# Performance work log

Measured on AMD Instinct MI355X. Metric: run time of the kernel, lower is better.

Reference implementation:

```python
import jax, jax.numpy as jnp
import numpy as np

IN_F, OUT_F = 4096, 4096
IN_Q, OUT_Q = IN_F // 4, OUT_F // 4


def setup_inputs() -> dict:
    key = jax.random.key(0)
    kx, kr, ki, kj, kk = jax.random.split(key, 5)
    std = 1.0 / np.sqrt(IN_F)
    x = jax.random.normal(kx, (4, 2048, IN_F), dtype=jnp.float32)
    Wr = std * jax.random.normal(kr, (OUT_Q, IN_Q), dtype=jnp.float32)
    Wi = std * jax.random.normal(ki, (OUT_Q, IN_Q), dtype=jnp.float32)
    Wj = std * jax.random.normal(kj, (OUT_Q, IN_Q), dtype=jnp.float32)
    Wk = std * jax.random.normal(kk, (OUT_Q, IN_Q), dtype=jnp.float32)
    bias = jnp.zeros((OUT_F,), dtype=jnp.float32)
    return {"x": x, "Wr": Wr, "Wi": Wi, "Wj": Wj, "Wk": Wk, "bias": bias}


def _hamilton_block(Wr, Wi, Wj, Wk):
    # Assemble the structured [4*out_q, 4*in_q] Hamilton block weight so the
    # whole op is ONE large GEMM instead of 16 small ones (same math).
    row_r = jnp.concatenate([Wr, -Wi, -Wj, -Wk], axis=1)
    row_i = jnp.concatenate([Wi,  Wr,  Wk, -Wj], axis=1)
    row_j = jnp.concatenate([Wj, -Wk,  Wr,  Wi], axis=1)
    row_k = jnp.concatenate([Wk,  Wj, -Wi,  Wr], axis=1)
    return jnp.concatenate([row_r, row_i, row_j, row_k], axis=0)  # [OUT_F, IN_F]


def reference(x, Wr, Wi, Wj, Wk, bias):
    W = _hamilton_block(Wr, Wi, Wj, Wk)
    # x: [B, S, IN_F] @ W.T -> [B, S, OUT_F]
    out = jnp.einsum('bsf,of->bso', x, W) + bias
    return out
```

## Files before the change

### kernel.cpp

```cpp
#include <hip/hip_runtime.h>
#include <hip/hip_bf16.h>


#define M_DIM 8192
#define N_DIM 4096
#define K_DIM 4096
#define BK 64
#define NT (K_DIM / BK)

typedef __attribute__((ext_vector_type(8))) short bf16x8;
typedef __attribute__((ext_vector_type(4))) float f32x4;
typedef __attribute__((ext_vector_type(8))) unsigned short ushort8;

static __device__ __forceinline__ unsigned short f2bf(float f) {
    unsigned int u = __float_as_uint(f);
    return (unsigned short)((u + 0x7fffu + ((u >> 16) & 1u)) >> 16);
}
static __device__ __forceinline__ unsigned short f2bf_sgn(float f, unsigned int sg) {
    unsigned int u = __float_as_uint(f) ^ sg;
    return (unsigned short)((u + 0x7fffu + ((u >> 16) & 1u)) >> 16);
}

__global__ __launch_bounds__(256) void cvt_x_kernel(const float* __restrict__ x,
                                                    unsigned short* __restrict__ xb) {
    int i = (blockIdx.x * 256 + threadIdx.x) * 8;
    f32x4 a = __builtin_nontemporal_load((const f32x4*)(x + i));
    f32x4 b = __builtin_nontemporal_load((const f32x4*)(x + i + 4));
    ushort8 o;
    o[0] = f2bf(a[0]); o[1] = f2bf(a[1]); o[2] = f2bf(a[2]); o[3] = f2bf(a[3]);
    o[4] = f2bf(b[0]); o[5] = f2bf(b[1]); o[6] = f2bf(b[2]); o[7] = f2bf(b[3]);
    *(ushort8*)(xb + i) = o;
}

__global__ __launch_bounds__(256) void prep_w_kernel(const float* __restrict__ Wr,
    const float* __restrict__ Wi, const float* __restrict__ Wj,
    const float* __restrict__ Wk, unsigned short* __restrict__ wb) {
    int row = blockIdx.x >> 1;
    int col = ((blockIdx.x & 1) * 256 + threadIdx.x) * 8;
    int p = row >> 10, q = col >> 10;
    int ci = p ^ q;
    const float* src = (ci == 0) ? Wr : (ci == 1) ? Wi : (ci == 2) ? Wj : Wk;
    unsigned int sg = ((0x428Eu >> (p * 4 + q)) & 1u) << 31;
    int so = (row & 1023) * 1024 + (col & 1023);
    f32x4 a = *(const f32x4*)(src + so);
    f32x4 b = *(const f32x4*)(src + so + 4);
    ushort8 o;
    o[0] = f2bf_sgn(a[0], sg); o[1] = f2bf_sgn(a[1], sg);
    o[2] = f2bf_sgn(a[2], sg); o[3] = f2bf_sgn(a[3], sg);
    o[4] = f2bf_sgn(b[0], sg); o[5] = f2bf_sgn(b[1], sg);
    o[6] = f2bf_sgn(b[2], sg); o[7] = f2bf_sgn(b[3], sg);
    *(ushort8*)(wb + row * 4096 + col) = o;
}

#define GLD16(gp, lp) __builtin_amdgcn_global_load_lds( \
    (const __attribute__((address_space(1))) void*)(gp), \
    (__attribute__((address_space(3))) void*)(lp), 16, 0, 0)

#define BAR() do { asm volatile("" ::: "memory"); \
                   __builtin_amdgcn_s_barrier(); \
                   asm volatile("" ::: "memory"); } while (0)
#define VM(n) asm volatile("s_waitcnt vmcnt(" #n ")" ::: "memory")

static __device__ __forceinline__ f32x4 MF(bf16x8 a, bf16x8 b, f32x4 c) {
    return __builtin_amdgcn_mfma_f32_16x16x32_bf16(a, b, c, 0, 0, 0);
}

__global__ __launch_bounds__(512, 2) void qgemm_bf16(
    const unsigned short* __restrict__ A, const unsigned short* __restrict__ B,
    const float* __restrict__ bias, float* __restrict__ out)
{
    __shared__ __align__(16) unsigned short Lsh[2][2][2][128 * 64];

    int bid = blockIdx.x;
    int cpx = gridDim.x >> 3;
    int wg  = (bid & 7) * cpx + (bid >> 3);
    int brow = (wg >> 4) * 256;
    int bcol = (wg & 15) * 256;

    int tid   = threadIdx.x;
    int lane  = tid & 63;
    int wid   = tid >> 6;
    int hA    = wid >> 2;
    int nb    = wid & 3;
    int hB    = nb >> 1;
    int rB0   = (nb & 1) << 6;
    int fr    = lane & 15;
    int fslot = lane >> 4;
    unsigned e = (unsigned)(fr & 7);

    const unsigned short* Ag = A + (size_t)brow * K_DIM;
    const unsigned short* Bg = B + (size_t)bcol * K_DIM;
    const char* LshB = (const char*)&Lsh[0][0][0][0];

    unsigned oA0 = (unsigned)hA * 16384u + (unsigned)fr * 128u
                 + ((((unsigned)fslot) ^ e) << 4);
    unsigned oA1 = oA0 ^ 64u;
    unsigned oB0 = 32768u + (unsigned)hB * 16384u
                 + (unsigned)(rB0 + fr) * 128u + ((((unsigned)fslot) ^ e) << 4);
    unsigned oB1 = oB0 ^ 64u;

    f32x4 acc[8][4] = {};

    auto stage = [&](int buf, int ab, int half, int t) {
        const unsigned short* g = (ab ? Bg : Ag) + (size_t)(half << 7) * K_DIM + t * BK;
        unsigned short* l = &Lsh[buf][ab][half][0];
        #pragma unroll
        for (int i = 0; i < 2; ++i) {
            int c = i * 512 + tid;
            int r = c >> 3, s = c & 7;
            GLD16(g + (size_t)r * K_DIM + ((s ^ (r & 7)) << 3), l + (c << 3));
        }
    };
    auto RD = [&](unsigned off) -> bf16x8 {
        return *(const bf16x8*)(LshB + off);
    };

#define CLUSTER(xa0, xa1, xb0, xb1, ra, rb)                                   \
    do {                                                                      \
        __builtin_amdgcn_s_setprio(1);                                        \
        _Pragma("unroll")                                                     \
        for (int ni = 0; ni < 4; ++ni) acc[ra][ni] = MF(xa0, bf0[ni], acc[ra][ni]); \
        _Pragma("unroll")                                                     \
        for (int ni = 0; ni < 4; ++ni) acc[rb][ni] = MF(xb0, bf0[ni], acc[rb][ni]); \
        _Pragma("unroll")                                                     \
        for (int ni = 0; ni < 4; ++ni) acc[ra][ni] = MF(xa1, bf1[ni], acc[ra][ni]); \
        _Pragma("unroll")                                                     \
        for (int ni = 0; ni < 4; ++ni) acc[rb][ni] = MF(xb1, bf1[ni], acc[rb][ni]); \
        __builtin_amdgcn_s_setprio(0);                                        \
    } while (0)

    stage(0, 0, 0, 0); stage(0, 0, 1, 0); stage(0, 1, 0, 0); stage(0, 1, 1, 0);
    stage(1, 1, 0, 1); stage(1, 1, 1, 1);
    VM(4); BAR();

    for (int t = 0; t < NT; ++t) {
        bf16x8 bf0[4], bf1[4];

        #pragma unroll
        for (int ni = 0; ni < 4; ++ni) {
            bf0[ni] = RD(oB0 + (unsigned)(ni * 2048));
            bf1[ni] = RD(oB1 + (unsigned)(ni * 2048));
        }
        bf16x8 p0a0 = RD(oA0), p0a1 = RD(oA1);
        bf16x8 p0b0 = RD(oA0 + 2048u), p0b1 = RD(oA1 + 2048u);
        if (t + 1 < NT) { stage((t & 1) ^ 1, 0, 0, t + 1); stage((t & 1) ^ 1, 0, 1, t + 1); }
        bf16x8 p1a0 = RD(oA0 + 4096u), p1a1 = RD(oA1 + 4096u);
        bf16x8 p1b0 = RD(oA0 + 6144u), p1b1 = RD(oA1 + 6144u);
        CLUSTER(p0a0, p0a1, p0b0, p0b1, 0, 1);
        BAR();

        if (t + 2 < NT) { stage(t & 1, 1, 0, t + 2); stage(t & 1, 1, 1, t + 2); }
        bf16x8 p2a0 = RD(oA0 + 8192u),  p2a1 = RD(oA1 + 8192u);
        bf16x8 p2b0 = RD(oA0 + 10240u), p2b1 = RD(oA1 + 10240u);
        CLUSTER(p1a0, p1a1, p1b0, p1b1, 2, 3);
        bf16x8 p3a0 = RD(oA0 + 12288u), p3a1 = RD(oA1 + 12288u);
        bf16x8 p3b0 = RD(oA0 + 14336u), p3b1 = RD(oA1 + 14336u);
        CLUSTER(p2a0, p2a1, p2b0, p2b1, 4, 5);
        CLUSTER(p3a0, p3a1, p3b0, p3b1, 6, 7);

        if (t < NT - 2) { VM(4); } else { VM(0); }
        BAR();
        oA0 ^= 0x10000u; oA1 ^= 0x10000u; oB0 ^= 0x10000u; oB1 ^= 0x10000u;
    }
#undef CLUSTER

    int cr = (lane >> 4) << 2;
    int cc = lane & 15;
    #pragma unroll
    for (int ni = 0; ni < 4; ++ni) {
        int col = bcol + nb * 64 + ni * 16 + cc;
        float bv = bias[col];
        #pragma unroll
        for (int mi = 0; mi < 8; ++mi) {
            int r0 = brow + hA * 128 + mi * 16 + cr;
            #pragma unroll
            for (int r = 0; r < 4; ++r)
                __builtin_nontemporal_store(acc[mi][ni][r] + bv,
                                            &out[(size_t)(r0 + r) * N_DIM + col]);
        }
    }
}

#define FBM 128
#define FBN 128
#define FBK 64
__global__ __launch_bounds__(256) void qgemm_fb(const float* __restrict__ x,
    const float* __restrict__ Wr, const float* __restrict__ Wi,
    const float* __restrict__ Wj, const float* __restrict__ Wk,
    const float* __restrict__ bias, float* __restrict__ out)
{
    __shared__ unsigned short As[FBM * FBK];
    __shared__ unsigned short Bs[FBN * FBK];

    int bid = blockIdx.x;
    int cpx = gridDim.x >> 3;
    int wg = (bid & 7) * cpx + (bid >> 3);
    int brow = (wg >> 5) * FBM;
    int bcol = (wg & 31) * FBN;

    int tid = threadIdx.x;
    int lane = tid & 63;
    int wv = tid >> 6;
    int wm = (wv >> 1) << 6;
    int wn = (wv & 1) << 6;
    int fr = lane & 15;
    int fk = (lane >> 4) << 3;

    int p = bcol >> 10;
    f32x4 acc[4][4] = {};

    for (int kt = 0; kt < K_DIM / FBK; ++kt) {
        int k0 = kt * FBK;
        int q = k0 >> 10;
        int ci = p ^ q;
        const float* wsrc = (ci == 0) ? Wr : (ci == 1) ? Wi : (ci == 2) ? Wj : Wk;
        unsigned int sg = ((0x428Eu >> (p * 4 + q)) & 1u) << 31;

        __syncthreads();
        #pragma unroll
        for (int i = 0; i < 4; ++i) {
            int c = i * 256 + tid;
            int row = c >> 3, colo = (c & 7) << 3;
            const float* s = x + (size_t)(brow + row) * K_DIM + k0 + colo;
            float4 a = *(const float4*)s;
            float4 b = *(const float4*)(s + 4);
            ushort8 o;
            o[0] = f2bf(a.x); o[1] = f2bf(a.y); o[2] = f2bf(a.z); o[3] = f2bf(a.w);
            o[4] = f2bf(b.x); o[5] = f2bf(b.y); o[6] = f2bf(b.z); o[7] = f2bf(b.w);
            *(ushort8*)(&As[c << 3]) = o;
        }
        #pragma unroll
        for (int i = 0; i < 4; ++i) {
            int c = i * 256 + tid;
            int row = c >> 3, colo = (c & 7) << 3;
            const float* s = wsrc + ((bcol + row) & 1023) * 1024 + ((k0 + colo) & 1023);
            float4 a = *(const float4*)s;
            float4 b = *(const float4*)(s + 4);
            ushort8 o;
            o[0] = f2bf_sgn(a.x, sg); o[1] = f2bf_sgn(a.y, sg);
            o[2] = f2bf_sgn(a.z, sg); o[3] = f2bf_sgn(a.w, sg);
            o[4] = f2bf_sgn(b.x, sg); o[5] = f2bf_sgn(b.y, sg);
            o[6] = f2bf_sgn(b.z, sg); o[7] = f2bf_sgn(b.w, sg);
            *(ushort8*)(&Bs[c << 3]) = o;
        }
        __syncthreads();

        #pragma unroll
        for (int ks = 0; ks < 2; ++ks) {
            bf16x8 af[4], bfr[4];
            #pragma unroll
            for (int m = 0; m < 4; ++m)
                af[m] = *(const bf16x8*)(&As[(wm + m * 16 + fr) * FBK + ks * 32 + fk]);
            #pragma unroll
            for (int n = 0; n < 4; ++n)
                bfr[n] = *(const bf16x8*)(&Bs[(wn + n * 16 + fr) * FBK + ks * 32 + fk]);
            #pragma unroll
            for (int m = 0; m < 4; ++m)
                #pragma unroll
                for (int n = 0; n < 4; ++n)
                    acc[m][n] = __builtin_amdgcn_mfma_f32_16x16x32_bf16(
                        af[m], bfr[n], acc[m][n], 0, 0, 0);
        }
    }

    int cr = (lane >> 4) << 2;
    int cc = lane & 15;
    #pragma unroll
    for (int n = 0; n < 4; ++n) {
        int col = bcol + wn + n * 16 + cc;
        float bv = bias[col];
        #pragma unroll
        for (int m = 0; m < 4; ++m) {
            int r0 = brow + wm + m * 16 + cr;
            #pragma unroll
            for (int r = 0; r < 4; ++r)
                out[(size_t)(r0 + r) * N_DIM + col] = acc[m][n][r] + bv;
        }
    }
}

extern "C" void kernel_launch(void* const* d_in, const int* in_sizes, int n_in,
                              void* d_out, int out_size, void* d_ws, size_t ws_size,
                              hipStream_t stream) {
    const float* x    = (const float*)d_in[0];
    const float* Wr   = (const float*)d_in[1];
    const float* Wi   = (const float*)d_in[2];
    const float* Wj   = (const float*)d_in[3];
    const float* Wk   = (const float*)d_in[4];
    const float* bias = (const float*)d_in[5];
    float* out = (float*)d_out;

    const size_t xb_bytes = (size_t)M_DIM * K_DIM * 2;
    const size_t wb_bytes = (size_t)N_DIM * K_DIM * 2;

    if (ws_size >= xb_bytes + wb_bytes) {
        unsigned short* xb = (unsigned short*)d_ws;
        unsigned short* wb = (unsigned short*)((char*)d_ws + xb_bytes);
        cvt_x_kernel<<<(M_DIM * K_DIM) / 2048, 256, 0, stream>>>(x, xb);
        prep_w_kernel<<<N_DIM * 2, 256, 0, stream>>>(Wr, Wi, Wj, Wk, wb);
        const int n_blocks = (M_DIM / 256) * (N_DIM / 256);
        qgemm_bf16<<<n_blocks, 512, 0, stream>>>(xb, wb, bias, out);
    } else {
        const int n_blocks = (M_DIM / FBM) * (N_DIM / FBN);
        qgemm_fb<<<n_blocks, 256, 0, stream>>>(x, Wr, Wi, Wj, Wk, bias, out);
    }
}
```

Baseline: 271.4 us.

## Use 16 waves per block with 64x64 per-wave tiles in bf16 GEMM

Doubles the workgroup to 1024 threads (16 waves in a 4x4 grid), so each wave computes a 64x64 output tile instead of 128x64, halving accumulator registers. LDS layout is flattened to full 256-row A/B tiles, staged by all threads, and A fragments are now read just in time inside each MFMA cluster. The goal is more waves to hide latency, at the cost of more LDS reads per MFMA and less register-level reuse. Launch bounds ask for 4 blocks per CU, which the 64 KB LDS footprint may not allow.

Measured after the change: 274.4 us. No clear change (+1.1%).

```diff
diff --git a/kernel.cpp b/kernel.cpp
--- a/kernel.cpp
+++ b/kernel.cpp
@@ -65,11 +65,11 @@
     return __builtin_amdgcn_mfma_f32_16x16x32_bf16(a, b, c, 0, 0, 0);
 }
 
-__global__ __launch_bounds__(512, 2) void qgemm_bf16(
+__global__ __launch_bounds__(1024, 4) void qgemm_bf16(
     const unsigned short* __restrict__ A, const unsigned short* __restrict__ B,
     const float* __restrict__ bias, float* __restrict__ out)
 {
-    __shared__ __align__(16) unsigned short Lsh[2][2][2][128 * 64];
+    __shared__ __align__(16) unsigned short Lsh[2][2][256 * 64];
 
     int bid = blockIdx.x;
     int cpx = gridDim.x >> 3;
@@ -80,33 +80,31 @@
     int tid   = threadIdx.x;
     int lane  = tid & 63;
     int wid   = tid >> 6;
-    int hA    = wid >> 2;
-    int nb    = wid & 3;
-    int hB    = nb >> 1;
-    int rB0   = (nb & 1) << 6;
+    int wm    = wid >> 2;
+    int wn    = wid & 3;
     int fr    = lane & 15;
     int fslot = lane >> 4;
     unsigned e = (unsigned)(fr & 7);
 
     const unsigned short* Ag = A + (size_t)brow * K_DIM;
     const unsigned short* Bg = B + (size_t)bcol * K_DIM;
-    const char* LshB = (const char*)&Lsh[0][0][0][0];
-
-    unsigned oA0 = (unsigned)hA * 16384u + (unsigned)fr * 128u
+    const char* LshB = (const char*)&Lsh[0][0][0];
+
+    unsigned oA0 = (unsigned)wm * 8192u + (unsigned)fr * 128u
                  + ((((unsigned)fslot) ^ e) << 4);
     unsigned oA1 = oA0 ^ 64u;
-    unsigned oB0 = 32768u + (unsigned)hB * 16384u
-                 + (unsigned)(rB0 + fr) * 128u + ((((unsigned)fslot) ^ e) << 4);
+    unsigned oB0 = 0x8000u + (unsigned)wn * 8192u + (unsigned)fr * 128u
+                 + ((((unsigned)fslot) ^ e) << 4);
     unsigned oB1 = oB0 ^ 64u;
 
-    f32x4 acc[8][4] = {};
-
-    auto stage = [&](int buf, int ab, int half, int t) {
-        const unsigned short* g = (ab ? Bg : Ag) + (size_t)(half << 7) * K_DIM + t * BK;
-        unsigned short* l = &Lsh[buf][ab][half][0];
+    f32x4 acc[4][4] = {};
+
+    auto stage = [&](int buf, int ab, int t) {
+        const unsigned short* g = (ab ? Bg : Ag) + t * BK;
+        unsigned short* l = &Lsh[buf][ab][0];
         #pragma unroll
         for (int i = 0; i < 2; ++i) {
-            int c = i * 512 + tid;
+            int c = i * 1024 + tid;
             int r = c >> 3, s = c & 7;
             GLD16(g + (size_t)r * K_DIM + ((s ^ (r & 7)) << 3), l + (c << 3));
         }
@@ -115,50 +113,40 @@
         return *(const bf16x8*)(LshB + off);
     };
 
-#define CLUSTER(xa0, xa1, xb0, xb1, ra, rb)                                   \
+#define CLUSTER(mi)                                                           \
     do {                                                                      \
+        bf16x8 a0 = RD(oA0 + (mi) * 2048u), a1 = RD(oA1 + (mi) * 2048u);      \
         __builtin_amdgcn_s_setprio(1);                                        \
         _Pragma("unroll")                                                     \
-        for (int ni = 0; ni < 4; ++ni) acc[ra][ni] = MF(xa0, bf0[ni], acc[ra][ni]); \
+        for (int ni = 0; ni < 4; ++ni) acc[mi][ni] = MF(a0, bf0[ni], acc[mi][ni]); \
         _Pragma("unroll")                                                     \
-        for (int ni = 0; ni < 4; ++ni) acc[rb][ni] = MF(xb0, bf0[ni], acc[rb][ni]); \
-        _Pragma("unroll")                                                     \
-        for (int ni = 0; ni < 4; ++ni) acc[ra][ni] = MF(xa1, bf1[ni], acc[ra][ni]); \
-        _Pragma("unroll")                                                     \
-        for (int ni = 0; ni < 4; ++ni) acc[rb][ni] = MF(xb1, bf1[ni], acc[rb][ni]); \
+        for (int ni = 0; ni < 4; ++ni) acc[mi][ni] = MF(a1, bf1[ni], acc[mi][ni]); \
         __builtin_amdgcn_s_setprio(0);                                        \
     } while (0)
 
-    stage(0, 0, 0, 0); stage(0, 0, 1, 0); stage(0, 1, 0, 0); stage(0, 1, 1, 0);
-    stage(1, 1, 0, 1); stage(1, 1, 1, 1);
-    VM(4); BAR();
+    bf16x8 bf0[4], bf1[4];
+
+    stage(0, 0, 0); stage(0, 1, 0); stage(1, 1, 1);
+    VM(2); BAR();
 
     for (int t = 0; t < NT; ++t) {
-        bf16x8 bf0[4], bf1[4];
-
+        int buf = t & 1;
+
+        if (t + 1 < NT) stage(buf ^ 1, 0, t + 1);
         #pragma unroll
         for (int ni = 0; ni < 4; ++ni) {
             bf0[ni] = RD(oB0 + (unsigned)(ni * 2048));
             bf1[ni] = RD(oB1 + (unsigned)(ni * 2048));
         }
-        bf16x8 p0a0 = RD(oA0), p0a1 = RD(oA1);
-        bf16x8 p0b0 = RD(oA0 + 2048u), p0b1 = RD(oA1 + 2048u);
-        if (t + 1 < NT) { stage((t & 1) ^ 1, 0, 0, t + 1); stage((t & 1) ^ 1, 0, 1, t + 1); }
-        bf16x8 p1a0 = RD(oA0 + 4096u), p1a1 = RD(oA1 + 4096u);
-        bf16x8 p1b0 = RD(oA0 + 6144u), p1b1 = RD(oA1 + 6144u);
-        CLUSTER(p0a0, p0a1, p0b0, p0b1, 0, 1);
+        CLUSTER(0);
         BAR();
 
-        if (t + 2 < NT) { stage(t & 1, 1, 0, t + 2); stage(t & 1, 1, 1, t + 2); }
-        bf16x8 p2a0 = RD(oA0 + 8192u),  p2a1 = RD(oA1 + 8192u);
-        bf16x8 p2b0 = RD(oA0 + 10240u), p2b1 = RD(oA1 + 10240u);
-        CLUSTER(p1a0, p1a1, p1b0, p1b1, 2, 3);
-        bf16x8 p3a0 = RD(oA0 + 12288u), p3a1 = RD(oA1 + 12288u);
-        bf16x8 p3b0 = RD(oA0 + 14336u), p3b1 = RD(oA1 + 14336u);
-        CLUSTER(p2a0, p2a1, p2b0, p2b1, 4, 5);
-        CLUSTER(p3a0, p3a1, p3b0, p3b1, 6, 7);
-
-        if (t < NT - 2) { VM(4); } else { VM(0); }
+        if (t + 2 < NT) stage(buf, 1, t + 2);
+        CLUSTER(1);
+        CLUSTER(2);
+        CLUSTER(3);
+
+        if (t < NT - 2) { VM(2); } else { VM(0); }
         BAR();
         oA0 ^= 0x10000u; oA1 ^= 0x10000u; oB0 ^= 0x10000u; oB1 ^= 0x10000u;
     }
@@ -168,11 +156,11 @@
     int cc = lane & 15;
     #pragma unroll
     for (int ni = 0; ni < 4; ++ni) {
-        int col = bcol + nb * 64 + ni * 16 + cc;
+        int col = bcol + wn * 64 + ni * 16 + cc;
         float bv = bias[col];
         #pragma unroll
-        for (int mi = 0; mi < 8; ++mi) {
-            int r0 = brow + hA * 128 + mi * 16 + cr;
+        for (int mi = 0; mi < 4; ++mi) {
+            int r0 = brow + wm * 64 + mi * 16 + cr;
             #pragma unroll
             for (int r = 0; r < 4; ++r)
                 __builtin_nontemporal_store(acc[mi][ni][r] + bv,
@@ -299,7 +287,7 @@
         cvt_x_kernel<<<(M_DIM * K_DIM) / 2048, 256, 0, stream>>>(x, xb);
         prep_w_kernel<<<N_DIM * 2, 256, 0, stream>>>(Wr, Wi, Wj, Wk, wb);
         const int n_blocks = (M_DIM / 256) * (N_DIM / 256);
-        qgemm_bf16<<<n_blocks, 512, 0, stream>>>(xb, wb, bias, out);
+        qgemm_bf16<<<n_blocks, 1024, 0, stream>>>(xb, wb, bias, out);
     } else {
         const int n_blocks = (M_DIM / FBM) * (N_DIM / FBN);
         qgemm_fb<<<n_blocks, 256, 0, stream>>>(x, Wr, Wi, Wj, Wk, bias, out);
```
